# Optimization experiments

Hardware: AMD Instinct MI355X
Metric: run time of the kernel (lower is better)

The kernel has to match this reference:

```python
import jax, jax.numpy as jnp
import numpy as np


def _maxpool2x2(t):
    # t: [B, C, H, W] -> [B, C, H//2, W//2]
    b, c, h, w = t.shape
    return t.reshape(b, c, h // 2, 2, w // 2, 2).max(axis=(3, 5))


def setup_inputs() -> dict:
    key = jax.random.key(0)
    ks = jax.random.split(key, 6)
    B, C, H, W = 16, 64, 64, 64
    x = jax.random.normal(ks[0], (B, C, H, W), dtype=jnp.float32)
    # 1x1 conv weights (no bias), stored as [out_ch, in_ch]
    s = 0.05
    W_theta = jax.random.normal(ks[1], (C // 8, C), dtype=jnp.float32) * s
    W_phi = jax.random.normal(ks[2], (C // 8, C), dtype=jnp.float32) * s
    W_g = jax.random.normal(ks[3], (C // 2, C), dtype=jnp.float32) * s
    W_attn = jax.random.normal(ks[4], (C, C // 2), dtype=jnp.float32) * s
    sigma = jnp.ones((1,), dtype=jnp.float32) * 0.5  # nonzero so attn path matters
    return {"x": x, "W_theta": W_theta, "W_phi": W_phi, "W_g": W_g,
            "W_attn": W_attn, "sigma": sigma}


def reference(x, W_theta, W_phi, W_g, W_attn, sigma):
    B, C, H, W = x.shape
    N = H * W
    M = N // 4
    # 1x1 convs are channel matmuls
    theta = jnp.einsum('oc,bchw->bohw', W_theta, x).reshape(B, C // 8, N)      # [B, C/8, N]
    phi = _maxpool2x2(jnp.einsum('oc,bchw->bohw', W_phi, x)).reshape(B, C // 8, M)  # [B, C/8, M]
    attn = jax.nn.softmax(jnp.einsum('bkn,bkm->bnm', theta, phi), axis=-1)    # [B, N, M]
    g = _maxpool2x2(jnp.einsum('oc,bchw->bohw', W_g, x)).reshape(B, C // 2, M)  # [B, C/2, M]
    attn_g = jnp.einsum('bgm,bnm->bgn', g, attn).reshape(B, C // 2, H, W)      # [B, C/2, H, W]
    attn_g = jnp.einsum('oc,bchw->bohw', W_attn, attn_g)                        # [B, C, H, W]
    return x + sigma * attn_g
```

## Files before the change

### kernel.cpp

```cpp
#include <hip/hip_runtime.h>
#include <hip/hip_bf16.h>

#define CC 64
#define NN 4096
#define MM 1024

typedef __attribute__((ext_vector_type(4))) short s4b;
typedef __attribute__((ext_vector_type(8))) short s8b;
typedef __attribute__((ext_vector_type(4))) float float4v;

__device__ inline unsigned short f2bf(float f) {
    union { float f; unsigned u; } v; v.f = f;
    unsigned r = v.u + 0x7fff + ((v.u >> 16) & 1);
    return (unsigned short)(r >> 16);
}

__device__ inline float4v mfma16(s4b a, s4b b, float4v c) {
#if __has_builtin(__builtin_amdgcn_mfma_f32_16x16x16bf16_1k)
    return __builtin_amdgcn_mfma_f32_16x16x16bf16_1k(a, b, c, 0, 0, 0);
#else
    float4v d;
    asm volatile("v_mfma_f32_16x16x16_bf16 %0, %1, %2, %3"
                 : "=v"(d) : "v"(a), "v"(b), "v"(c));
    return d;
#endif
}

__device__ inline float4v mfma32(s8b a, s8b b, float4v c) {
#if __has_builtin(__builtin_amdgcn_mfma_f32_16x16x32_bf16)
    return __builtin_amdgcn_mfma_f32_16x16x32_bf16(a, b, c, 0, 0, 0);
#else
    float4v d;
    asm volatile("v_mfma_f32_16x16x32_bf16 %0, %1, %2, %3"
                 : "=v"(d) : "v"(a), "v"(b), "v"(c));
    return d;
#endif
}

__global__ __launch_bounds__(256) void prep_kernel(
    const float* __restrict__ x,
    const float* __restrict__ Wth,
    const float* __restrict__ Wph,
    const float* __restrict__ Wg,
    unsigned short* __restrict__ thT,
    unsigned short* __restrict__ phiP,
    unsigned short* __restrict__ gP)
{
    __shared__ float wt[64 * 48];
    __shared__ float buf[128 * 49];

    const int tid  = threadIdx.x;
    const int b    = blockIdx.y;
    const int hp   = blockIdx.x;
    const int pix  = tid & 127;
    const int half = tid >> 7;

    for (int idx = tid; idx < 64 * 48; idx += 256) {
        const int c = idx / 48, j = idx % 48;
        float v;
        if (j < 8)       v = Wth[j * 64 + c];
        else if (j < 16) v = Wph[(j - 8) * 64 + c];
        else             v = Wg[(j - 16) * 64 + c];
        wt[c * 48 + j] = v;
    }
    __syncthreads();

    const int n = (2 * hp + (pix >> 6)) * 64 + (pix & 63);
    const float* xb = x + (size_t)b * CC * NN + (size_t)half * 32 * NN + n;

    float acc[48];
#pragma unroll
    for (int j = 0; j < 48; ++j) acc[j] = 0.f;

#pragma unroll
    for (int c0 = 0; c0 < 32; c0 += 16) {
        float xv[16];
#pragma unroll
        for (int u = 0; u < 16; ++u) xv[u] = xb[(size_t)(c0 + u) * NN];
#pragma unroll
        for (int u = 0; u < 16; ++u) {
            const float* wrow = &wt[(half * 32 + c0 + u) * 48];
#pragma unroll
            for (int j = 0; j < 48; ++j) acc[j] += wrow[j] * xv[u];
        }
    }

    if (half == 1) {
#pragma unroll
        for (int j = 0; j < 48; ++j) buf[pix * 49 + j] = acc[j];
    }
    __syncthreads();

    if (half == 0) {
#pragma unroll
        for (int j = 0; j < 48; ++j) acc[j] += buf[pix * 49 + j];
        union { unsigned short s[8]; uint4 v; } pk;
#pragma unroll
        for (int j = 0; j < 8; ++j) pk.s[j] = f2bf(acc[j] * 1.44269504f);
        *(uint4*)&thT[((size_t)b * NN + n) * 8] = pk.v;
#pragma unroll
        for (int j = 0; j < 40; ++j) buf[pix * 49 + j] = acc[8 + j];
    }
    __syncthreads();

    for (int idx = tid; idx < 1280; idx += 256) {
        const int pm = idx & 31;
        const int j  = idx >> 5;
        const int p00 = 2 * pm, p10 = 64 + 2 * pm;
        const float v = fmaxf(fmaxf(buf[p00 * 49 + j], buf[(p00 + 1) * 49 + j]),
                              fmaxf(buf[p10 * 49 + j], buf[(p10 + 1) * 49 + j]));
        const int m = hp * 32 + pm;
        if (j < 8) phiP[((size_t)b * MM + m) * 8 + j] = f2bf(v);
        else       gP[((size_t)b * 32 + (j - 8)) * MM + m] = f2bf(v);
    }
}

__global__ __launch_bounds__(256) void attn_mfma(
    const unsigned short* __restrict__ thT,
    const unsigned short* __restrict__ phiP,
    const unsigned short* __restrict__ gP,
    const float* __restrict__ x,
    const float* __restrict__ Wa,
    const float* __restrict__ sigma,
    float* __restrict__ out)
{
    constexpr int GP = 264;
    constexpr int OBP = 40;

    __shared__ __align__(16) union {
        struct {
            unsigned short phi[256 * 8 + 16];
            unsigned short g[32 * GP];
        } m;
        unsigned short obb[64 * OBP];
    } sh;

    const int tid  = threadIdx.x;
    const int lane = tid & 63;
    const int wv   = tid >> 6;
    const int c15  = lane & 15;
    const int quad = lane >> 4;
    const int b    = blockIdx.y;
    const int n0   = blockIdx.x * 64;

    union { unsigned short s[8]; s8b v; } wfrag;
    {
        const float* wr = Wa + (wv * 16 + c15) * 32 + quad * 8;
        const float4 w0 = *(const float4*)wr;
        const float4 w1 = *(const float4*)(wr + 4);
        wfrag.s[0] = f2bf(w0.x); wfrag.s[1] = f2bf(w0.y);
        wfrag.s[2] = f2bf(w0.z); wfrag.s[3] = f2bf(w0.w);
        wfrag.s[4] = f2bf(w1.x); wfrag.s[5] = f2bf(w1.y);
        wfrag.s[6] = f2bf(w1.z); wfrag.s[7] = f2bf(w1.w);
    }

    s4b zero4 = {0, 0, 0, 0};
    s4b bth = zero4;
    if (quad < 2) {
        union { uint2 u; s4b s; } t;
        t.u = *(const uint2*)&thT[((size_t)b * NN + n0 + wv * 16 + c15) * 8 + quad * 4];
        bth = t.s;
    }

    float4v acc0 = {0.f, 0.f, 0.f, 0.f};
    float4v acc1 = {0.f, 0.f, 0.f, 0.f};
    float zacc = 0.f;

    for (int ch = 0; ch < 4; ++ch) {
        __syncthreads();
        {
            const int r  = tid & 7;
            const int q3 = (tid >> 3) & 3;
            const int slot = (tid & ~31) | ((r >> 2) << 4) | (q3 << 2) | (r & 3);
            *(uint4*)&sh.m.phi[slot * 8] =
                *(const uint4*)&phiP[((size_t)b * MM + ch * 256 + tid) * 8];
            if (tid < 2) {
                uint4 z4; z4.x = z4.y = z4.z = z4.w = 0u;
                *(uint4*)&sh.m.phi[256 * 8 + tid * 8] = z4;
            }
        }
#pragma unroll
        for (int it = 0; it < 4; ++it) {
            const int idx = tid + 256 * it;
            const int row = idx >> 5, c32 = idx & 31;
            *(uint4*)&sh.m.g[row * GP + c32 * 8] =
                *(const uint4*)&gP[((size_t)b * 32 + row) * MM + ch * 256 + c32 * 8];
        }
        __syncthreads();

        const unsigned short* pA  = &sh.m.phi[c15 * 8 + quad * 4];
        const unsigned short* pg0 = &sh.m.g[c15 * GP + quad * 8];
        const unsigned short* pg1 = pg0 + 16 * GP;

#pragma unroll
        for (int g32 = 0; g32 < 8; ++g32) {
            union { uint2 u; s4b s; } apA, apB;
            apA.u = *(const uint2*)&pA[g32 * 256];
            apB.u = *(const uint2*)&pA[g32 * 256 + 128];

            float4v cz = {0.f, 0.f, 0.f, 0.f};
            float4v scA = mfma16(apA.s, bth, cz);
            float4v scB = mfma16(apB.s, bth, cz);

            union { float f; unsigned u; } a0, a1, a2, a3, b0, b1, b2, b3;
            a0.f = __builtin_amdgcn_exp2f(scA[0]);
            a1.f = __builtin_amdgcn_exp2f(scA[1]);
            a2.f = __builtin_amdgcn_exp2f(scA[2]);
            a3.f = __builtin_amdgcn_exp2f(scA[3]);
            b0.f = __builtin_amdgcn_exp2f(scB[0]);
            b1.f = __builtin_amdgcn_exp2f(scB[1]);
            b2.f = __builtin_amdgcn_exp2f(scB[2]);
            b3.f = __builtin_amdgcn_exp2f(scB[3]);
            zacc += ((a0.f + a1.f) + (a2.f + a3.f)) +
                    ((b0.f + b1.f) + (b2.f + b3.f));
            union { uint4 u; s8b s; } pa;
            pa.u.x = __builtin_amdgcn_perm(a1.u, a0.u, 0x07060302u);
            pa.u.y = __builtin_amdgcn_perm(a3.u, a2.u, 0x07060302u);
            pa.u.z = __builtin_amdgcn_perm(b1.u, b0.u, 0x07060302u);
            pa.u.w = __builtin_amdgcn_perm(b3.u, b2.u, 0x07060302u);

            union { uint4 u; s8b s; } bg0, bg1;
            bg0.u = *(const uint4*)&pg0[g32 * 32];
            bg1.u = *(const uint4*)&pg1[g32 * 32];

            acc0 = mfma32(pa.s, bg0.s, acc0);
            acc1 = mfma32(pa.s, bg1.s, acc1);
        }
    }

    float z = zacc;
    z += __shfl_xor(z, 16, 64);
    z += __shfl_xor(z, 32, 64);
    const float rzq = __builtin_amdgcn_rcpf(z);

    __syncthreads();

#pragma unroll
    for (int r = 0; r < 4; ++r) {
        const float rz = __shfl(rzq, quad * 4 + r, 64);
        const int ql = wv * 16 + quad * 4 + r;
        sh.obb[ql * OBP + c15]      = f2bf(acc0[r] * rz);
        sh.obb[ql * OBP + 16 + c15] = f2bf(acc1[r] * rz);
    }
    __syncthreads();

    const float sg = sigma[0];
#pragma unroll
    for (int t = 0; t < 4; ++t) {
        union { uint4 u; s8b s; } bo;
        bo.u = *(const uint4*)&sh.obb[(t * 16 + c15) * OBP + quad * 8];
        float4v cz = {0.f, 0.f, 0.f, 0.f};
        float4v oc = mfma32(wfrag.v, bo.s, cz);
#pragma unroll
        for (int r = 0; r < 4; ++r) {
            const size_t oi = ((size_t)b * CC + wv * 16 + quad * 4 + r) * NN
                              + n0 + t * 16 + c15;
            out[oi] = x[oi] + sg * oc[r];
        }
    }
}

extern "C" void kernel_launch(void* const* d_in, const int* in_sizes, int n_in,
                              void* d_out, int out_size, void* d_ws, size_t ws_size,
                              hipStream_t stream) {
    const float* x      = (const float*)d_in[0];
    const float* W_th   = (const float*)d_in[1];
    const float* W_ph   = (const float*)d_in[2];
    const float* W_g    = (const float*)d_in[3];
    const float* W_attn = (const float*)d_in[4];
    const float* sigma  = (const float*)d_in[5];
    float* out = (float*)d_out;

    const int B = 16;
    unsigned short* thT  = (unsigned short*)d_ws;
    unsigned short* phiP = thT + (size_t)B * NN * 8;
    unsigned short* gP   = phiP + (size_t)B * MM * 8;

    prep_kernel<<<dim3(32, 16), 256, 0, stream>>>(x, W_th, W_ph, W_g,
                                                  thT, phiP, gP);
    attn_mfma<<<dim3(64, 16), 256, 0, stream>>>(thT, phiP, gP, x,
                                                W_attn, sigma, out);
}
```

Baseline: 105.2 us.

## Double query tile per attention block and restructure prep projection with pixel pairs

```diff
diff --git a/kernel.cpp b/kernel.cpp
--- a/kernel.cpp
+++ b/kernel.cpp
@@ -46,72 +46,105 @@
     unsigned short* __restrict__ phiP,
     unsigned short* __restrict__ gP)
 {
-    __shared__ float wt[64 * 48];
-    __shared__ float buf[128 * 49];
+    __shared__ __align__(16) float wtg[4 * 776];
+    __shared__ __align__(16) float pbuf[32 * 40];
 
     const int tid  = threadIdx.x;
     const int b    = blockIdx.y;
     const int hp   = blockIdx.x;
-    const int pix  = tid & 127;
-    const int half = tid >> 7;
-
-    for (int idx = tid; idx < 64 * 48; idx += 256) {
+    const int lane = tid & 63;
+    const int w    = tid >> 6;
+    const int h2   = lane >> 4;
+    const int sl   = lane & 15;
+    const int row  = w >> 1;
+    const int cp   = (w & 1) * 16 + sl;
+
+    for (int idx = tid; idx < 3072; idx += 256) {
         const int c = idx / 48, j = idx % 48;
         float v;
         if (j < 8)       v = Wth[j * 64 + c];
         else if (j < 16) v = Wph[(j - 8) * 64 + c];
         else             v = Wg[(j - 16) * 64 + c];
-        wt[c * 48 + j] = v;
+        wtg[(c >> 4) * 776 + (c & 15) * 48 + j] = v;
     }
     __syncthreads();
 
-    const int n = (2 * hp + (pix >> 6)) * 64 + (pix & 63);
-    const float* xb = x + (size_t)b * CC * NN + (size_t)half * 32 * NN + n;
-
-    float acc[48];
-#pragma unroll
-    for (int j = 0; j < 48; ++j) acc[j] = 0.f;
-
-#pragma unroll
-    for (int c0 = 0; c0 < 32; c0 += 16) {
-        float xv[16];
-#pragma unroll
-        for (int u = 0; u < 16; ++u) xv[u] = xb[(size_t)(c0 + u) * NN];
-#pragma unroll
-        for (int u = 0; u < 16; ++u) {
-            const float* wrow = &wt[(half * 32 + c0 + u) * 48];
-#pragma unroll
-            for (int j = 0; j < 48; ++j) acc[j] += wrow[j] * xv[u];
-        }
-    }
-
-    if (half == 1) {
-#pragma unroll
-        for (int j = 0; j < 48; ++j) buf[pix * 49 + j] = acc[j];
+    const int n = (2 * hp + row) * 64 + 2 * cp;
+    const float* xb = x + (size_t)b * CC * NN + (size_t)(h2 * 16) * NN + n;
+
+    float2 xv[16];
+#pragma unroll
+    for (int u = 0; u < 16; ++u) xv[u] = *(const float2*)&xb[(size_t)u * NN];
+
+    float ax[48], ay[48];
+#pragma unroll
+    for (int j = 0; j < 48; ++j) { ax[j] = 0.f; ay[j] = 0.f; }
+
+    const float* wr0 = &wtg[h2 * 776];
+#pragma unroll
+    for (int u = 0; u < 16; ++u) {
+        const float* wrow = wr0 + u * 48;
+        const float2 xu = xv[u];
+#pragma unroll
+        for (int j = 0; j < 48; ++j) {
+            const float wv_ = wrow[j];
+            ax[j] = fmaf(wv_, xu.x, ax[j]);
+            ay[j] = fmaf(wv_, xu.y, ay[j]);
+        }
+    }
+
+#pragma unroll
+    for (int j = 0; j < 48; ++j) {
+        ax[j] += __shfl_xor(ax[j], 16, 64);
+        ay[j] += __shfl_xor(ay[j], 16, 64);
+        ax[j] += __shfl_xor(ax[j], 32, 64);
+        ay[j] += __shfl_xor(ay[j], 32, 64);
+    }
+
+    if (h2 == 0) {
+        union { unsigned short s[16]; uint4 v[2]; } pk;
+#pragma unroll
+        for (int j = 0; j < 8; ++j) {
+            pk.s[j]     = f2bf(ax[j] * 1.44269504f);
+            pk.s[8 + j] = f2bf(ay[j] * 1.44269504f);
+        }
+        uint4* dst = (uint4*)&thT[((size_t)b * NN + n) * 8];
+        dst[0] = pk.v[0]; dst[1] = pk.v[1];
+    }
+
+    float hm[40];
+#pragma unroll
+    for (int j = 0; j < 40; ++j) hm[j] = fmaxf(ax[8 + j], ay[8 + j]);
+
+    if (row == 1 && h2 == 1) {
+#pragma unroll
+        for (int j4 = 0; j4 < 10; ++j4) {
+            float4 t;
+            t.x = hm[j4 * 4 + 0]; t.y = hm[j4 * 4 + 1];
+            t.z = hm[j4 * 4 + 2]; t.w = hm[j4 * 4 + 3];
+            *(float4*)&pbuf[cp * 40 + j4 * 4] = t;
+        }
     }
     __syncthreads();
 
-    if (half == 0) {
-#pragma unroll
-        for (int j = 0; j < 48; ++j) acc[j] += buf[pix * 49 + j];
-        union { unsigned short s[8]; uint4 v; } pk;
-#pragma unroll
-        for (int j = 0; j < 8; ++j) pk.s[j] = f2bf(acc[j] * 1.44269504f);
-        *(uint4*)&thT[((size_t)b * NN + n) * 8] = pk.v;
-#pragma unroll
-        for (int j = 0; j < 40; ++j) buf[pix * 49 + j] = acc[8 + j];
-    }
-    __syncthreads();
-
-    for (int idx = tid; idx < 1280; idx += 256) {
-        const int pm = idx & 31;
-        const int j  = idx >> 5;
-        const int p00 = 2 * pm, p10 = 64 + 2 * pm;
-        const float v = fmaxf(fmaxf(buf[p00 * 49 + j], buf[(p00 + 1) * 49 + j]),
-                              fmaxf(buf[p10 * 49 + j], buf[(p10 + 1) * 49 + j]));
-        const int m = hp * 32 + pm;
-        if (j < 8) phiP[((size_t)b * MM + m) * 8 + j] = f2bf(v);
-        else       gP[((size_t)b * 32 + (j - 8)) * MM + m] = f2bf(v);
+    if (row == 0 && h2 >= 2) {
+        const int m = hp * 32 + cp;
+        if (h2 == 2) {
+            union { unsigned short s[8]; uint4 v; } pk;
+#pragma unroll
+            for (int j = 0; j < 8; ++j)
+                pk.s[j] = f2bf(fmaxf(hm[j], pbuf[cp * 40 + j]));
+            *(uint4*)&phiP[((size_t)b * MM + m) * 8] = pk.v;
+#pragma unroll
+            for (int j = 8; j < 24; ++j)
+                gP[((size_t)b * 32 + (j - 8)) * MM + m] =
+                    f2bf(fmaxf(hm[j], pbuf[cp * 40 + j]));
+        } else {
+#pragma unroll
+            for (int j = 24; j < 40; ++j)
+                gP[((size_t)b * 32 + (j - 8)) * MM + m] =
+                    f2bf(fmaxf(hm[j], pbuf[cp * 40 + j]));
+        }
     }
 }
 
@@ -132,7 +165,7 @@
             unsigned short phi[256 * 8 + 16];
             unsigned short g[32 * GP];
         } m;
-        unsigned short obb[64 * OBP];
+        unsigned short obb[128 * OBP];
     } sh;
 
     const int tid  = threadIdx.x;
@@ -141,7 +174,7 @@
     const int c15  = lane & 15;
     const int quad = lane >> 4;
     const int b    = blockIdx.y;
-    const int n0   = blockIdx.x * 64;
+    const int n0   = blockIdx.x * 128;
 
     union { unsigned short s[8]; s8b v; } wfrag;
     {
@@ -155,16 +188,20 @@
     }
 
     s4b zero4 = {0, 0, 0, 0};
-    s4b bth = zero4;
+    s4b bthA = zero4, bthB = zero4;
     if (quad < 2) {
         union { uint2 u; s4b s; } t;
-        t.u = *(const uint2*)&thT[((size_t)b * NN + n0 + wv * 16 + c15) * 8 + quad * 4];
-        bth = t.s;
-    }
-
-    float4v acc0 = {0.f, 0.f, 0.f, 0.f};
-    float4v acc1 = {0.f, 0.f, 0.f, 0.f};
-    float zacc = 0.f;
+        t.u = *(const uint2*)&thT[((size_t)b * NN + n0 + wv * 32 + c15) * 8 + quad * 4];
+        bthA = t.s;
+        t.u = *(const uint2*)&thT[((size_t)b * NN + n0 + wv * 32 + 16 + c15) * 8 + quad * 4];
+        bthB = t.s;
+    }
+
+    float4v accA0 = {0.f, 0.f, 0.f, 0.f};
+    float4v accA1 = {0.f, 0.f, 0.f, 0.f};
+    float4v accB0 = {0.f, 0.f, 0.f, 0.f};
+    float4v accB1 = {0.f, 0.f, 0.f, 0.f};
+    float zaccA = 0.f, zaccB = 0.f;
 
     for (int ch = 0; ch < 4; ++ch) {
         __syncthreads();
@@ -182,9 +219,9 @@
 #pragma unroll
         for (int it = 0; it < 4; ++it) {
             const int idx = tid + 256 * it;
-            const int row = idx >> 5, c32 = idx & 31;
-            *(uint4*)&sh.m.g[row * GP + c32 * 8] =
-                *(const uint4*)&gP[((size_t)b * 32 + row) * MM + ch * 256 + c32 * 8];
+            const int grow = idx >> 5, c32 = idx & 31;
+            *(uint4*)&sh.m.g[grow * GP + c32 * 8] =
+                *(const uint4*)&gP[((size_t)b * 32 + grow) * MM + ch * 256 + c32 * 8];
         }
         __syncthreads();
 
@@ -199,54 +236,81 @@
             apB.u = *(const uint2*)&pA[g32 * 256 + 128];
 
             float4v cz = {0.f, 0.f, 0.f, 0.f};
-            float4v scA = mfma16(apA.s, bth, cz);
-            float4v scB = mfma16(apB.s, bth, cz);
+            float4v sAlo = mfma16(apA.s, bthA, cz);
+            float4v sAhi = mfma16(apB.s, bthA, cz);
+            float4v sBlo = mfma16(apA.s, bthB, cz);
+            float4v sBhi = mfma16(apB.s, bthB, cz);
 
             union { float f; unsigned u; } a0, a1, a2, a3, b0, b1, b2, b3;
-            a0.f = __builtin_amdgcn_exp2f(scA[0]);
-            a1.f = __builtin_amdgcn_exp2f(scA[1]);
-            a2.f = __builtin_amdgcn_exp2f(scA[2]);
-            a3.f = __builtin_amdgcn_exp2f(scA[3]);
-            b0.f = __builtin_amdgcn_exp2f(scB[0]);
-            b1.f = __builtin_amdgcn_exp2f(scB[1]);
-            b2.f = __builtin_amdgcn_exp2f(scB[2]);
-            b3.f = __builtin_amdgcn_exp2f(scB[3]);
-            zacc += ((a0.f + a1.f) + (a2.f + a3.f)) +
-                    ((b0.f + b1.f) + (b2.f + b3.f));
-            union { uint4 u; s8b s; } pa;
-            pa.u.x = __builtin_amdgcn_perm(a1.u, a0.u, 0x07060302u);
-            pa.u.y = __builtin_amdgcn_perm(a3.u, a2.u, 0x07060302u);
-            pa.u.z = __builtin_amdgcn_perm(b1.u, b0.u, 0x07060302u);
-            pa.u.w = __builtin_amdgcn_perm(b3.u, b2.u, 0x07060302u);
+            a0.f = __builtin_amdgcn_exp2f(sAlo[0]);
+            a1.f = __builtin_amdgcn_exp2f(sAlo[1]);
+            a2.f = __builtin_amdgcn_exp2f(sAlo[2]);
+            a3.f = __builtin_amdgcn_exp2f(sAlo[3]);
+            b0.f = __builtin_amdgcn_exp2f(sAhi[0]);
+            b1.f = __builtin_amdgcn_exp2f(sAhi[1]);
+            b2.f = __builtin_amdgcn_exp2f(sAhi[2]);
+            b3.f = __builtin_amdgcn_exp2f(sAhi[3]);
+            zaccA += ((a0.f + a1.f) + (a2.f + a3.f)) +
+                     ((b0.f + b1.f) + (b2.f + b3.f));
+            union { uint4 u; s8b s; } paA;
+            paA.u.x = __builtin_amdgcn_perm(a1.u, a0.u, 0x07060302u);
+            paA.u.y = __builtin_amdgcn_perm(a3.u, a2.u, 0x07060302u);
+            paA.u.z = __builtin_amdgcn_perm(b1.u, b0.u, 0x07060302u);
+            paA.u.w = __builtin_amdgcn_perm(b3.u, b2.u, 0x07060302u);
+
+            a0.f = __builtin_amdgcn_exp2f(sBlo[0]);
+            a1.f = __builtin_amdgcn_exp2f(sBlo[1]);
+            a2.f = __builtin_amdgcn_exp2f(sBlo[2]);
+            a3.f = __builtin_amdgcn_exp2f(sBlo[3]);
+            b0.f = __builtin_amdgcn_exp2f(sBhi[0]);
+            b1.f = __builtin_amdgcn_exp2f(sBhi[1]);
+            b2.f = __builtin_amdgcn_exp2f(sBhi[2]);
+            b3.f = __builtin_amdgcn_exp2f(sBhi[3]);
+            zaccB += ((a0.f + a1.f) + (a2.f + a3.f)) +
+                     ((b0.f + b1.f) + (b2.f + b3.f));
+            union { uint4 u; s8b s; } paB;
+            paB.u.x = __builtin_amdgcn_perm(a1.u, a0.u, 0x07060302u);
+            paB.u.y = __builtin_amdgcn_perm(a3.u, a2.u, 0x07060302u);
+            paB.u.z = __builtin_amdgcn_perm(b1.u, b0.u, 0x07060302u);
+            paB.u.w = __builtin_amdgcn_perm(b3.u, b2.u, 0x07060302u);
 
             union { uint4 u; s8b s; } bg0, bg1;
             bg0.u = *(const uint4*)&pg0[g32 * 32];
             bg1.u = *(const uint4*)&pg1[g32 * 32];
 
-            acc0 = mfma32(pa.s, bg0.s, acc0);
-            acc1 = mfma32(pa.s, bg1.s, acc1);
-        }
-    }
-
-    float z = zacc;
-    z += __shfl_xor(z, 16, 64);
-    z += __shfl_xor(z, 32, 64);
-    const float rzq = __builtin_amdgcn_rcpf(z);
+            accA0 = mfma32(paA.s, bg0.s, accA0);
+            accA1 = mfma32(paA.s, bg1.s, accA1);
+            accB0 = mfma32(paB.s, bg0.s, accB0);
+            accB1 = mfma32(paB.s, bg1.s, accB1);
+        }
+    }
+
+    float zA = zaccA, zB = zaccB;
+    zA += __shfl_xor(zA, 16, 64);
+    zA += __shfl_xor(zA, 32, 64);
+    zB += __shfl_xor(zB, 16, 64);
+    zB += __shfl_xor(zB, 32, 64);
+    const float rzqA = __builtin_amdgcn_rcpf(zA);
+    const float rzqB = __builtin_amdgcn_rcpf(zB);
 
     __syncthreads();
 
 #pragma unroll
     for (int r = 0; r < 4; ++r) {
-        const float rz = __shfl(rzq, quad * 4 + r, 64);
-        const int ql = wv * 16 + quad * 4 + r;
-        sh.obb[ql * OBP + c15]      = f2bf(acc0[r] * rz);
-        sh.obb[ql * OBP + 16 + c15] = f2bf(acc1[r] * rz);
+        const float rzA = __shfl(rzqA, quad * 4 + r, 64);
+        const float rzB = __shfl(rzqB, quad * 4 + r, 64);
+        const int qlA = wv * 32 + quad * 4 + r;
+        const int qlB = qlA + 16;
+        sh.obb[qlA * OBP + c15]      = f2bf(accA0[r] * rzA);
+        sh.obb[qlA * OBP + 16 + c15] = f2bf(accA1[r] * rzA);
+        sh.obb[qlB * OBP + c15]      = f2bf(accB0[r] * rzB);
+        sh.obb[qlB * OBP + 16 + c15] = f2bf(accB1[r] * rzB);
     }
     __syncthreads();
 
     const float sg = sigma[0];
 #pragma unroll
-    for (int t = 0; t < 4; ++t) {
+    for (int t = 0; t < 8; ++t) {
         union { uint4 u; s8b s; } bo;
         bo.u = *(const uint4*)&sh.obb[(t * 16 + c15) * OBP + quad * 8];
         float4v cz = {0.f, 0.f, 0.f, 0.f};
@@ -278,6 +342,6 @@
 
     prep_kernel<<<dim3(32, 16), 256, 0, stream>>>(x, W_th, W_ph, W_g,
                                                   thT, phiP, gP);
-    attn_mfma<<<dim3(64, 16), 256, 0, stream>>>(thT, phiP, gP, x,
+    attn_mfma<<<dim3(32, 16), 256, 0, stream>>>(thT, phiP, gP, x,
                                                 W_attn, sigma, out);
 }
```

Result: no change. 106.2 us (+0.9%).
